# Performance work log

Hardware: AMD Instinct MI355X
Metric: run time of the kernel (lower is better)

## Reference

```python
import jax, jax.numpy as jnp
import numpy as np

N = 50000
E = 1600000
IN_DIM = 256
HID = 128
EPS = 1e-5


def _bn(x, gamma, beta):
    # BatchNorm1d forward in training mode: biased batch stats
    mean = jnp.mean(x, axis=0)
    var = jnp.mean((x - mean) ** 2, axis=0)
    return (x - mean) * jax.lax.rsqrt(var + EPS) * gamma + beta


def _sage(x, edge_index, Wl, bl, Wr):
    # PyG SAGEConv with mean aggregation:
    #   out = lin_l(mean_{j in N(i)} x_j) + lin_r(x_i)
    src, dst = edge_index[0], edge_index[1]
    agg = jax.ops.segment_sum(x[src], dst, num_segments=N)          # [N, H]
    cnt = jax.ops.segment_sum(jnp.ones((src.shape[0],), x.dtype), dst, num_segments=N)
    mean = agg / jnp.maximum(cnt, 1.0)[:, None]
    return mean @ Wl + bl + x @ Wr


def setup_inputs() -> dict:
    key = jax.random.key(0)
    ks = jax.random.split(key, 16)
    s_in = 1.0 / np.sqrt(IN_DIM)
    s_h = 1.0 / np.sqrt(HID)
    return {
        "x": jax.random.normal(ks[0], (N, IN_DIM), jnp.float32),
        "edge_index": jax.random.randint(ks[1], (2, E), 0, N, jnp.int32),
        # input_linear: Linear(IN_DIM, HID) + BN
        "W_in": jax.random.uniform(ks[2], (IN_DIM, HID), jnp.float32, -s_in, s_in),
        "b_in": jax.random.uniform(ks[3], (HID,), jnp.float32, -s_in, s_in),
        "g1": jnp.ones((HID,), jnp.float32), "be1": jnp.zeros((HID,), jnp.float32),
        # hidden_linear: Linear(HID, HID) + BN
        "W_hid": jax.random.uniform(ks[4], (HID, HID), jnp.float32, -s_h, s_h),
        "b_hid": jax.random.uniform(ks[5], (HID,), jnp.float32, -s_h, s_h),
        "g2": jnp.ones((HID,), jnp.float32), "be2": jnp.zeros((HID,), jnp.float32),
        # graph_conv1: SAGEConv(HID, HID) + BN
        "Wl1": jax.random.uniform(ks[6], (HID, HID), jnp.float32, -s_h, s_h),
        "bl1": jax.random.uniform(ks[7], (HID,), jnp.float32, -s_h, s_h),
        "Wr1": jax.random.uniform(ks[8], (HID, HID), jnp.float32, -s_h, s_h),
        "g3": jnp.ones((HID,), jnp.float32), "be3": jnp.zeros((HID,), jnp.float32),
        # graph_conv2: SAGEConv(HID, HID) + BN
        "Wl2": jax.random.uniform(ks[9], (HID, HID), jnp.float32, -s_h, s_h),
        "bl2": jax.random.uniform(ks[10], (HID,), jnp.float32, -s_h, s_h),
        "Wr2": jax.random.uniform(ks[11], (HID, HID), jnp.float32, -s_h, s_h),
        "g4": jnp.ones((HID,), jnp.float32), "be4": jnp.zeros((HID,), jnp.float32),
    }


def reference(x, edge_index, W_in, b_in, g1, be1, W_hid, b_hid, g2, be2,
              Wl1, bl1, Wr1, g3, be3, Wl2, bl2, Wr2, g4, be4):
    feat = jax.nn.relu(_bn(x @ W_in + b_in, g1, be1))
    feat = jax.nn.relu(_bn(feat @ W_hid + b_hid, g2, be2))
    out = _bn(_sage(feat, edge_index, Wl1, bl1, Wr1), g3, be3)
    out = _bn(_sage(out, edge_index, Wl2, bl2, Wr2), g4, be4)
    return (feat, out)
```

## Files before the change

kernel.cpp:

```cpp
#include <hip/hip_runtime.h>
#include <stdint.h>

#define NN 50000
#define EE 1600000
#define IN_DIMC 256
#define HIDC 128
#define EPSC 1e-5f

#define NB 196
#define GA 512
#define CHUNK 3125
#define STILE_SHIFT 13
#define NKEY 2048

typedef unsigned short ushort_t;
typedef __attribute__((ext_vector_type(8))) short short8;
typedef __attribute__((ext_vector_type(4))) float floatx4;

static __device__ inline ushort_t f2bf(float f) {
    unsigned int u = __float_as_uint(f);
    u = u + 0x7fffu + ((u >> 16) & 1u);
    return (ushort_t)(u >> 16);
}
static __device__ inline unsigned int pack2(float a, float b) {
    return (unsigned int)f2bf(a) | ((unsigned int)f2bf(b) << 16);
}
static __device__ inline float bf2f(unsigned int bits16) {
    return __uint_as_float(bits16 << 16);
}

__global__ __launch_bounds__(256) void tcvt_all_kernel(
    const float* __restrict__ W_in, const float* __restrict__ W_hid,
    const float* __restrict__ Wl1, const float* __restrict__ Wr1,
    const float* __restrict__ Wl2, const float* __restrict__ Wr2,
    ushort_t* __restrict__ Wt_in, ushort_t* __restrict__ Wt_hid,
    ushort_t* __restrict__ Wtl1, ushort_t* __restrict__ Wtr1,
    ushort_t* __restrict__ Wtl2, ushort_t* __restrict__ Wtr2)
{
    const int idx = blockIdx.x * 256 + threadIdx.x;
    if (idx < 32768) {
        const int n = idx >> 8;
        const int k = idx & 255;
        Wt_in[idx] = f2bf(W_in[(size_t)k * 128 + n]);
    } else if (idx < 32768 + 5 * 16384) {
        const int r = idx - 32768;
        const int seg = r / 16384;
        const int j = r - seg * 16384;
        const int n = j >> 7;
        const int k = j & 127;
        const float* W; ushort_t* Wt;
        switch (seg) {
            case 0: W = W_hid; Wt = Wt_hid; break;
            case 1: W = Wl1;  Wt = Wtl1;  break;
            case 2: W = Wr1;  Wt = Wtr1;  break;
            case 3: W = Wl2;  Wt = Wtl2;  break;
            default: W = Wr2; Wt = Wtr2;  break;
        }
        Wt[j] = f2bf(W[(size_t)k * 128 + n]);
    }
}

__global__ __launch_bounds__(256) void mfma_gemm_kernel(
    const void* __restrict__ A1, const ushort_t* __restrict__ Wt1, int K1, int a1type,
    const void* __restrict__ A2, const ushort_t* __restrict__ Wt2, int K2,
    const float* __restrict__ bias, float* __restrict__ C, int M,
    const float* __restrict__ preStats, const float* __restrict__ preG,
    const float* __restrict__ preBe, float* __restrict__ outStats)
{
    __shared__ ushort_t Bs[128 * 136];
    __shared__ __align__(16) float aArr[128], bArr[128];
    __shared__ float red_s[4][128], red_q[4][128];

    const int t    = threadIdx.x;
    const int lane = t & 63;
    const int wave = t >> 6;
    const int quad = lane >> 4;
    const int l15  = lane & 15;
    const int row0 = blockIdx.x * 128 + wave * 32;
    const int doAffine = (preStats != nullptr);

    if (doAffine && t < 128) {
        const float invM = 1.0f / (float)M;
        const float mean = preStats[t] * invM;
        float var = preStats[128 + t] * invM - mean * mean;
        if (var < 0.0f) var = 0.0f;
        const float s = preG[t] / sqrtf(var + EPSC);
        aArr[t] = s;
        bArr[t] = preBe[t] - mean * s;
    }
    if (doAffine) __syncthreads();

    floatx4 acc[2][8];
    #pragma unroll
    for (int i = 0; i < 2; i++)
        #pragma unroll
        for (int j = 0; j < 8; j++)
            acc[i][j] = (floatx4){0.0f, 0.0f, 0.0f, 0.0f};

    const int ksq = quad * 8;
    bool firstChunk = true;

    for (int s = 0; s < 2; s++) {
        const void*     A     = s ? A2  : A1;
        const ushort_t* Wt    = s ? Wt2 : Wt1;
        const int       K     = s ? K2  : K1;
        const int       atype = s ? 1   : a1type;
        if (A == nullptr) continue;

        for (int kc = 0; kc < K; kc += 128) {
            if (!firstChunk) __syncthreads();
            firstChunk = false;

            #pragma unroll
            for (int p = 0; p < 8; p++) {
                const int idx = p * 256 + t;
                const int n   = idx >> 4;
                const int c0  = (idx & 15) * 8;
                *(uint4*)(Bs + n * 136 + c0) =
                    *(const uint4*)(Wt + (size_t)n * K + kc + c0);
            }
            __syncthreads();

            short8 afrag[2][4];
            if (atype == 1) {
                const ushort_t* Ab = (const ushort_t*)A;
                #pragma unroll
                for (int mt = 0; mt < 2; mt++) {
                    int gr = row0 + mt * 16 + l15;
                    if (gr > M - 1) gr = M - 1;
                    const size_t base = (size_t)gr * K + kc + ksq;
                    #pragma unroll
                    for (int ks = 0; ks < 4; ks++)
                        afrag[mt][ks] = *(const short8*)(Ab + base + ks * 32);
                }
            } else {
                const float* Af = (const float*)A;
                #pragma unroll
                for (int mt = 0; mt < 2; mt++) {
                    int gr = row0 + mt * 16 + l15;
                    if (gr > M - 1) gr = M - 1;
                    const size_t base = (size_t)gr * K + kc + ksq;
                    #pragma unroll
                    for (int ks = 0; ks < 4; ks++) {
                        float4 v0 = *(const float4*)(Af + base + ks * 32);
                        float4 v1 = *(const float4*)(Af + base + ks * 32 + 4);
                        if (doAffine && s == 0) {
                            const int k0 = ks * 32 + ksq;
                            const float4 sa0 = *(const float4*)(aArr + k0);
                            const float4 sb0 = *(const float4*)(bArr + k0);
                            const float4 sa1 = *(const float4*)(aArr + k0 + 4);
                            const float4 sb1 = *(const float4*)(bArr + k0 + 4);
                            v0.x = fmaxf(sa0.x * v0.x + sb0.x, 0.0f);
                            v0.y = fmaxf(sa0.y * v0.y + sb0.y, 0.0f);
                            v0.z = fmaxf(sa0.z * v0.z + sb0.z, 0.0f);
                            v0.w = fmaxf(sa0.w * v0.w + sb0.w, 0.0f);
                            v1.x = fmaxf(sa1.x * v1.x + sb1.x, 0.0f);
                            v1.y = fmaxf(sa1.y * v1.y + sb1.y, 0.0f);
                            v1.z = fmaxf(sa1.z * v1.z + sb1.z, 0.0f);
                            v1.w = fmaxf(sa1.w * v1.w + sb1.w, 0.0f);
                        }
                        uint4 w;
                        w.x = pack2(v0.x, v0.y);
                        w.y = pack2(v0.z, v0.w);
                        w.z = pack2(v1.x, v1.y);
                        w.w = pack2(v1.z, v1.w);
                        afrag[mt][ks] = __builtin_bit_cast(short8, w);
                    }
                }
            }

            #pragma unroll
            for (int ks = 0; ks < 4; ks++) {
                const int ko = ks * 32 + ksq;
                short8 b[8];
                #pragma unroll
                for (int j = 0; j < 8; j++)
                    b[j] = *(const short8*)(Bs + (j * 16 + l15) * 136 + ko);
                #pragma unroll
                for (int mt = 0; mt < 2; mt++) {
                    #pragma unroll
                    for (int j = 0; j < 8; j++)
                        acc[mt][j] = __builtin_amdgcn_mfma_f32_16x16x32_bf16(
                            afrag[mt][ks], b[j], acc[mt][j], 0, 0, 0);
                }
            }
        }
    }

    float s_[8], q_[8];
    #pragma unroll
    for (int j = 0; j < 8; j++) { s_[j] = 0.0f; q_[j] = 0.0f; }

    #pragma unroll
    for (int j = 0; j < 8; j++) {
        const int col = j * 16 + l15;
        const float bv = bias[col];
        #pragma unroll
        for (int mt = 0; mt < 2; mt++) {
            const int rbase = row0 + mt * 16 + quad * 4;
            #pragma unroll
            for (int reg = 0; reg < 4; reg++) {
                const float val = acc[mt][j][reg] + bv;
                const int r_ = rbase + reg;
                if (r_ < M) {
                    C[(size_t)r_ * HIDC + col] = val;
                    s_[j] += val;
                    q_[j] += val * val;
                }
            }
        }
    }
    #pragma unroll
    for (int j = 0; j < 8; j++) {
        s_[j] += __shfl_xor(s_[j], 16, 64);
        s_[j] += __shfl_xor(s_[j], 32, 64);
        q_[j] += __shfl_xor(q_[j], 16, 64);
        q_[j] += __shfl_xor(q_[j], 32, 64);
    }
    if (quad == 0) {
        #pragma unroll
        for (int j = 0; j < 8; j++) {
            red_s[wave][j * 16 + l15] = s_[j];
            red_q[wave][j * 16 + l15] = q_[j];
        }
    }
    __syncthreads();
    if (t < 128) {
        const float S = red_s[0][t] + red_s[1][t] + red_s[2][t] + red_s[3][t];
        const float Q = red_q[0][t] + red_q[1][t] + red_q[2][t] + red_q[3][t];
        atomicAdd(&outStats[t], S);
        atomicAdd(&outStats[128 + t], Q);
    }
}

__global__ __launch_bounds__(256) void bn_apply_kernel(
    const float* __restrict__ src, float* __restrict__ dstF,
    ushort_t* __restrict__ dstB, const float* __restrict__ stats,
    const float* __restrict__ gamma, const float* __restrict__ beta,
    int relu, int M)
{
    __shared__ float sc[128], sh[128];
    const int t = threadIdx.x;
    if (t < 128) {
        const float invM = 1.0f / (float)M;
        const float mean = stats[t] * invM;
        float var = stats[128 + t] * invM - mean * mean;
        if (var < 0.0f) var = 0.0f;
        const float s = gamma[t] / sqrtf(var + EPSC);
        sc[t] = s;
        sh[t] = beta[t] - mean * s;
    }
    __syncthreads();

    const int total4 = M * HIDC / 4;
    for (int i = blockIdx.x * 256 + t; i < total4; i += gridDim.x * 256) {
        float4 v = ((const float4*)src)[i];
        const int c = (i * 4) & 127;
        v.x = v.x * sc[c]     + sh[c];
        v.y = v.y * sc[c + 1] + sh[c + 1];
        v.z = v.z * sc[c + 2] + sh[c + 2];
        v.w = v.w * sc[c + 3] + sh[c + 3];
        if (relu) {
            v.x = fmaxf(v.x, 0.0f); v.y = fmaxf(v.y, 0.0f);
            v.z = fmaxf(v.z, 0.0f); v.w = fmaxf(v.w, 0.0f);
        }
        if (dstF) ((float4*)dstF)[i] = v;
        if (dstB) {
            uint2 w;
            w.x = pack2(v.x, v.y);
            w.y = pack2(v.z, v.w);
            *(uint2*)(dstB + (size_t)i * 4) = w;
        }
    }
}

__global__ __launch_bounds__(256) void bucket_hist_kernel(
    const int* __restrict__ dstArr, int* __restrict__ hist2D)
{
    __shared__ int hist[NB];
    const int t = threadIdx.x;
    for (int i = t; i < NB; i += 256) hist[i] = 0;
    __syncthreads();
    const int e0 = blockIdx.x * CHUNK;
    const int e1 = e0 + CHUNK;
    for (int e = e0 + t; e < e1; e += 256)
        atomicAdd(&hist[dstArr[e] >> 8], 1);
    __syncthreads();
    for (int i = t; i < NB; i += 256)
        hist2D[(size_t)i * GA + blockIdx.x] = hist[i];
}

__global__ __launch_bounds__(256) void bucket_offsets_kernel(
    int* __restrict__ hist2D, int* __restrict__ bucketBase, int* __restrict__ rowp)
{
    __shared__ int wtot[4];
    const int t = threadIdx.x;
    int tot = 0;
    if (t < NB) {
        int4* p = (int4*)(hist2D + (size_t)t * GA);
        int s = 0;
        for (int i = 0; i < GA / 4; i++) {
            int4 h = p[i];
            int4 o;
            o.x = s; s += h.x;
            o.y = s; s += h.y;
            o.z = s; s += h.z;
            o.w = s; s += h.w;
            p[i] = o;
        }
        tot = s;
    }
    const int lane = t & 63, w = t >> 6;
    int x = tot;
    #pragma unroll
    for (int off = 1; off < 64; off <<= 1) {
        const int y = __shfl_up(x, off);
        if (lane >= off) x += y;
    }
    if (lane == 63) wtot[w] = x;
    __syncthreads();
    int woff = 0;
    #pragma unroll
    for (int j = 0; j < 4; j++) if (j < w) woff += wtot[j];
    const int excl = x + woff - tot;
    if (t < NB) bucketBase[t] = excl;
    if (t == 0) { bucketBase[NB] = EE; rowp[NN] = EE; }
}

__global__ __launch_bounds__(256) void bucket_scatter_kernel(
    const int* __restrict__ srcArr, const int* __restrict__ dstArr,
    const int* __restrict__ hist2D, const int* __restrict__ bucketBase,
    int2* __restrict__ ebuf)
{
    __shared__ int cur[NB];
    const int t = threadIdx.x;
    for (int i = t; i < NB; i += 256)
        cur[i] = bucketBase[i] + hist2D[(size_t)i * GA + blockIdx.x];
    __syncthreads();
    const int e0 = blockIdx.x * CHUNK;
    const int e1 = e0 + CHUNK;
    for (int e = e0 + t; e < e1; e += 256) {
        const int d = dstArr[e];
        const int s = srcArr[e];
        const int p = atomicAdd(&cur[d >> 8], 1);
        ebuf[p] = make_int2(s, d);
    }
}

__global__ __launch_bounds__(256) void fine_sort_kernel(
    const int2* __restrict__ ebuf, const int* __restrict__ bucketBase,
    int* __restrict__ rowp, int* __restrict__ col)
{
    __shared__ int cnt[NKEY];
    __shared__ int wtot[4];
    const int b = blockIdx.x;
    const int t = threadIdx.x;
    const int bb0 = bucketBase[b];
    const int bb1 = bucketBase[b + 1];
    #pragma unroll
    for (int i = 0; i < 8; i++) cnt[t * 8 + i] = 0;
    __syncthreads();
    for (int e = bb0 + t; e < bb1; e += 256) {
        const int2 sd = ebuf[e];
        const int key = ((sd.y & 255) << 3) | (sd.x >> STILE_SHIFT);
        atomicAdd(&cnt[key], 1);
    }
    __syncthreads();
    int loc[8];
    int tot = 0;
    #pragma unroll
    for (int i = 0; i < 8; i++) { loc[i] = tot; tot += cnt[t * 8 + i]; }
    const int lane = t & 63, w = t >> 6;
    int x = tot;
    #pragma unroll
    for (int off = 1; off < 64; off <<= 1) {
        const int y = __shfl_up(x, off);
        if (lane >= off) x += y;
    }
    if (lane == 63) wtot[w] = x;
    __syncthreads();
    int woff = 0;
    #pragma unroll
    for (int j = 0; j < 4; j++) if (j < w) woff += wtot[j];
    const int excl = x + woff - tot;
    const int node = b * 256 + t;
    if (node < NN) rowp[node] = bb0 + excl;
    __syncthreads();
    #pragma unroll
    for (int i = 0; i < 8; i++) cnt[t * 8 + i] = excl + loc[i];
    __syncthreads();
    for (int e = bb0 + t; e < bb1; e += 256) {
        const int2 sd = ebuf[e];
        const int key = ((sd.y & 255) << 3) | (sd.x >> STILE_SHIFT);
        const int p = atomicAdd(&cnt[key], 1);
        col[bb0 + p] = sd.x;
    }
}

__global__ __launch_bounds__(256) void agg_kernel(
    const ushort_t* __restrict__ F, const int* __restrict__ row_ptr,
    const int* __restrict__ col, ushort_t* __restrict__ Mout)
{
    const int lane = threadIdx.x & 63;
    const int wave = blockIdx.x * (blockDim.x >> 6) + (threadIdx.x >> 6);
    const int nwaves = gridDim.x * (blockDim.x >> 6);
    const int coff = lane * 2;

    for (int n = wave; n < NN; n += nwaves) {
        const int b = __builtin_amdgcn_readfirstlane(row_ptr[n]);
        const int e = __builtin_amdgcn_readfirstlane(row_ptr[n + 1]);
        const int deg = e - b;
        float accx = 0.0f, accy = 0.0f;
        int j = b;
        for (; j + 8 <= e; j += 8) {
            const int s0 = col[j + 0];
            const int s1 = col[j + 1];
            const int s2 = col[j + 2];
            const int s3 = col[j + 3];
            const int s4 = col[j + 4];
            const int s5 = col[j + 5];
            const int s6 = col[j + 6];
            const int s7 = col[j + 7];
            const unsigned int v0 = *(const unsigned int*)(F + (size_t)s0 * HIDC + coff);
            const unsigned int v1 = *(const unsigned int*)(F + (size_t)s1 * HIDC + coff);
            const unsigned int v2 = *(const unsigned int*)(F + (size_t)s2 * HIDC + coff);
            const unsigned int v3 = *(const unsigned int*)(F + (size_t)s3 * HIDC + coff);
            const unsigned int v4 = *(const unsigned int*)(F + (size_t)s4 * HIDC + coff);
            const unsigned int v5 = *(const unsigned int*)(F + (size_t)s5 * HIDC + coff);
            const unsigned int v6 = *(const unsigned int*)(F + (size_t)s6 * HIDC + coff);
            const unsigned int v7 = *(const unsigned int*)(F + (size_t)s7 * HIDC + coff);
            accx += bf2f(v0 & 0xffffu) + bf2f(v1 & 0xffffu) + bf2f(v2 & 0xffffu)
                  + bf2f(v3 & 0xffffu) + bf2f(v4 & 0xffffu) + bf2f(v5 & 0xffffu)
                  + bf2f(v6 & 0xffffu) + bf2f(v7 & 0xffffu);
            accy += bf2f(v0 >> 16) + bf2f(v1 >> 16) + bf2f(v2 >> 16)
                  + bf2f(v3 >> 16) + bf2f(v4 >> 16) + bf2f(v5 >> 16)
                  + bf2f(v6 >> 16) + bf2f(v7 >> 16);
        }
        for (; j < e; j++) {
            const int s = col[j];
            const unsigned int v = *(const unsigned int*)(F + (size_t)s * HIDC + coff);
            accx += bf2f(v & 0xffffu);
            accy += bf2f(v >> 16);
        }
        const float inv = 1.0f / (float)(deg > 1 ? deg : 1);
        *(unsigned int*)(Mout + (size_t)n * HIDC + coff) =
            pack2(accx * inv, accy * inv);
    }
}

extern "C" void kernel_launch(void* const* d_in, const int* in_sizes, int n_in,
                              void* d_out, int out_size, void* d_ws, size_t ws_size,
                              hipStream_t stream)
{
    const float* x     = (const float*)d_in[0];
    const int*   ei    = (const int*)  d_in[1];
    const float* W_in  = (const float*)d_in[2];
    const float* b_in  = (const float*)d_in[3];
    const float* g1    = (const float*)d_in[4];
    const float* be1   = (const float*)d_in[5];
    const float* W_hid = (const float*)d_in[6];
    const float* b_hid = (const float*)d_in[7];
    const float* g2    = (const float*)d_in[8];
    const float* be2   = (const float*)d_in[9];
    const float* Wl1   = (const float*)d_in[10];
    const float* bl1   = (const float*)d_in[11];
    const float* Wr1   = (const float*)d_in[12];
    const float* g3    = (const float*)d_in[13];
    const float* be3   = (const float*)d_in[14];
    const float* Wl2   = (const float*)d_in[15];
    const float* bl2   = (const float*)d_in[16];
    const float* Wr2   = (const float*)d_in[17];
    const float* g4    = (const float*)d_in[18];
    const float* be4   = (const float*)d_in[19];

    const int* srcArr = ei;
    const int* dstArr = ei + EE;

    char* ws = (char*)d_ws;
    float*    bufA      = (float*)ws;    ws += (size_t)NN * HIDC * sizeof(float);
    float*    bufB      = (float*)ws;    ws += (size_t)NN * HIDC * sizeof(float);
    ushort_t* featB16   = (ushort_t*)ws; ws += (size_t)NN * HIDC * sizeof(ushort_t);
    ushort_t* o3B16     = (ushort_t*)ws; ws += (size_t)NN * HIDC * sizeof(ushort_t);
    ushort_t* aggB16    = (ushort_t*)ws; ws += (size_t)NN * HIDC * sizeof(ushort_t);
    float*    stats     = (float*)ws;    ws += 4 * 256 * sizeof(float);
    int*      hist2D    = (int*)ws;      ws += (size_t)NB * GA * sizeof(int);
    int*      bucketBase= (int*)ws;      ws += (NB + 4) * sizeof(int);
    int*      rowp      = (int*)ws;      ws += (size_t)(NN + 4) * sizeof(int);
    int*      colIdx    = (int*)ws;      ws += (size_t)EE * sizeof(int);
    int2*     ebuf      = (int2*)ws;     ws += (size_t)EE * sizeof(int2);
    ushort_t* Wt_in     = (ushort_t*)ws; ws += 128 * 256 * sizeof(ushort_t);
    ushort_t* Wt_hid    = (ushort_t*)ws; ws += 128 * 128 * sizeof(ushort_t);
    ushort_t* Wtl1      = (ushort_t*)ws; ws += 128 * 128 * sizeof(ushort_t);
    ushort_t* Wtr1      = (ushort_t*)ws; ws += 128 * 128 * sizeof(ushort_t);
    ushort_t* Wtl2      = (ushort_t*)ws; ws += 128 * 128 * sizeof(ushort_t);
    ushort_t* Wtr2      = (ushort_t*)ws; ws += 128 * 128 * sizeof(ushort_t);

    float* out0 = (float*)d_out;
    float* out1 = out0 + (size_t)NN * HIDC;

    hipMemsetAsync(stats, 0, 4 * 256 * sizeof(float), stream);

    tcvt_all_kernel<<<448, 256, 0, stream>>>(W_in, W_hid, Wl1, Wr1, Wl2, Wr2,
                                             Wt_in, Wt_hid, Wtl1, Wtr1, Wtl2, Wtr2);

    bucket_hist_kernel<<<GA, 256, 0, stream>>>(dstArr, hist2D);
    bucket_offsets_kernel<<<1, 256, 0, stream>>>(hist2D, bucketBase, rowp);
    bucket_scatter_kernel<<<GA, 256, 0, stream>>>(srcArr, dstArr, hist2D,
                                                  bucketBase, ebuf);
    fine_sort_kernel<<<NB, 256, 0, stream>>>(ebuf, bucketBase, rowp, colIdx);

    const int gemmGrid = (NN + 127) / 128;

    mfma_gemm_kernel<<<gemmGrid, 256, 0, stream>>>(
        x, Wt_in, IN_DIMC, 0, nullptr, nullptr, 0,
        b_in, bufA, NN, nullptr, nullptr, nullptr, stats + 0);

    mfma_gemm_kernel<<<gemmGrid, 256, 0, stream>>>(
        bufA, Wt_hid, HIDC, 0, nullptr, nullptr, 0,
        b_hid, bufB, NN, stats + 0, g1, be1, stats + 256);

    bn_apply_kernel<<<1024, 256, 0, stream>>>(bufB, out0, featB16,
                                              stats + 256, g2, be2, 1, NN);

    agg_kernel<<<4096, 256, 0, stream>>>(featB16, rowp, colIdx, aggB16);
    mfma_gemm_kernel<<<gemmGrid, 256, 0, stream>>>(
        aggB16, Wtl1, HIDC, 1, featB16, Wtr1, HIDC,
        bl1, bufA, NN, nullptr, nullptr, nullptr, stats + 512);

    bn_apply_kernel<<<1024, 256, 0, stream>>>(bufA, nullptr, o3B16,
                                              stats + 512, g3, be3, 0, NN);

    agg_kernel<<<4096, 256, 0, stream>>>(o3B16, rowp, colIdx, aggB16);
    mfma_gemm_kernel<<<gemmGrid, 256, 0, stream>>>(
        aggB16, Wtl2, HIDC, 1, o3B16, Wtr2, HIDC,
        bl2, bufB, NN, nullptr, nullptr, nullptr, stats + 768);

    bn_apply_kernel<<<1024, 256, 0, stream>>>(bufB, out1, nullptr,
                                              stats + 768, g4, be4, 0, NN);
}
```

Baseline: 441.5 us.

## Shrink GEMM tiles, drop LDS B staging, pack edges and intermediates to 16-bit

The GEMM now processes 64 rows per block with one 16-row tile per wave. It reads weight fragments directly from global memory instead of staging them through shared memory, which removes the block barriers. The first GEMM writes a bf16 intermediate, and the second GEMM applies BN+ReLU on the bf16 input, which halves that round-trip traffic at some precision cost. Edge buffers pack src/dst into 32 bits and column indices into 16-bit shorts; this relies on N fitting in 16 bits. The aggregation kernel now launches one wave per node instead of a grid-stride loop.

```diff
diff --git a/kernel.cpp b/kernel.cpp
--- a/kernel.cpp
+++ b/kernel.cpp
@@ -60,14 +60,14 @@
     }
 }
 
-__global__ __launch_bounds__(256) void mfma_gemm_kernel(
+__global__ __launch_bounds__(256, 4) void mfma_gemm_kernel(
     const void* __restrict__ A1, const ushort_t* __restrict__ Wt1, int K1, int a1type,
     const void* __restrict__ A2, const ushort_t* __restrict__ Wt2, int K2,
-    const float* __restrict__ bias, float* __restrict__ C, int M,
+    const float* __restrict__ bias, float* __restrict__ Cf, ushort_t* __restrict__ Cb,
+    int M,
     const float* __restrict__ preStats, const float* __restrict__ preG,
     const float* __restrict__ preBe, float* __restrict__ outStats)
 {
-    __shared__ ushort_t Bs[128 * 136];
     __shared__ __align__(16) float aArr[128], bArr[128];
     __shared__ float red_s[4][128], red_q[4][128];
 
@@ -76,29 +76,30 @@
     const int wave = t >> 6;
     const int quad = lane >> 4;
     const int l15  = lane & 15;
-    const int row0 = blockIdx.x * 128 + wave * 32;
+    const int row0 = blockIdx.x * 64 + wave * 16;
     const int doAffine = (preStats != nullptr);
 
-    if (doAffine && t < 128) {
-        const float invM = 1.0f / (float)M;
-        const float mean = preStats[t] * invM;
-        float var = preStats[128 + t] * invM - mean * mean;
-        if (var < 0.0f) var = 0.0f;
-        const float s = preG[t] / sqrtf(var + EPSC);
-        aArr[t] = s;
-        bArr[t] = preBe[t] - mean * s;
-    }
-    if (doAffine) __syncthreads();
-
-    floatx4 acc[2][8];
-    #pragma unroll
-    for (int i = 0; i < 2; i++)
-        #pragma unroll
-        for (int j = 0; j < 8; j++)
-            acc[i][j] = (floatx4){0.0f, 0.0f, 0.0f, 0.0f};
+    if (doAffine) {
+        if (t < 128) {
+            const float invM = 1.0f / (float)M;
+            const float mean = preStats[t] * invM;
+            float var = preStats[128 + t] * invM - mean * mean;
+            if (var < 0.0f) var = 0.0f;
+            const float s = preG[t] / sqrtf(var + EPSC);
+            aArr[t] = s;
+            bArr[t] = preBe[t] - mean * s;
+        }
+        __syncthreads();
+    }
+
+    floatx4 acc[8];
+    #pragma unroll
+    for (int j = 0; j < 8; j++)
+        acc[j] = (floatx4){0.0f, 0.0f, 0.0f, 0.0f};
 
     const int ksq = quad * 8;
-    bool firstChunk = true;
+    int gr = row0 + l15;
+    if (gr > M - 1) gr = M - 1;
 
     for (int s = 0; s < 2; s++) {
         const void*     A     = s ? A2  : A1;
@@ -108,81 +109,74 @@
         if (A == nullptr) continue;
 
         for (int kc = 0; kc < K; kc += 128) {
-            if (!firstChunk) __syncthreads();
-            firstChunk = false;
-
-            #pragma unroll
-            for (int p = 0; p < 8; p++) {
-                const int idx = p * 256 + t;
-                const int n   = idx >> 4;
-                const int c0  = (idx & 15) * 8;
-                *(uint4*)(Bs + n * 136 + c0) =
-                    *(const uint4*)(Wt + (size_t)n * K + kc + c0);
-            }
-            __syncthreads();
-
-            short8 afrag[2][4];
+            short8 afrag[4];
             if (atype == 1) {
                 const ushort_t* Ab = (const ushort_t*)A;
+                const size_t base = (size_t)gr * K + kc + ksq;
                 #pragma unroll
-                for (int mt = 0; mt < 2; mt++) {
-                    int gr = row0 + mt * 16 + l15;
-                    if (gr > M - 1) gr = M - 1;
-                    const size_t base = (size_t)gr * K + kc + ksq;
+                for (int ks = 0; ks < 4; ks++)
+                    afrag[ks] = *(const short8*)(Ab + base + ks * 32);
+                if (doAffine && s == 0) {
                     #pragma unroll
-                    for (int ks = 0; ks < 4; ks++)
-                        afrag[mt][ks] = *(const short8*)(Ab + base + ks * 32);
+                    for (int ks = 0; ks < 4; ks++) {
+                        const int k0 = kc + ks * 32 + ksq;
+                        uint4 u = __builtin_bit_cast(uint4, afrag[ks]);
+                        uint4 w;
+                        unsigned int* up = (unsigned int*)&u;
+                        unsigned int* wp = (unsigned int*)&w;
+                        #pragma unroll
+                        for (int h = 0; h < 4; h++) {
+                            const float lo = bf2f(up[h] & 0xffffu);
+                            const float hi = bf2f(up[h] >> 16);
+                            const float flo = fmaxf(aArr[k0 + h * 2]     * lo + bArr[k0 + h * 2],     0.0f);
+                            const float fhi = fmaxf(aArr[k0 + h * 2 + 1] * hi + bArr[k0 + h * 2 + 1], 0.0f);
+                            wp[h] = pack2(flo, fhi);
+                        }
+                        afrag[ks] = __builtin_bit_cast(short8, w);
+                    }
                 }
             } else {
                 const float* Af = (const float*)A;
+                const size_t base = (size_t)gr * K + kc + ksq;
                 #pragma unroll
-                for (int mt = 0; mt < 2; mt++) {
-                    int gr = row0 + mt * 16 + l15;
-                    if (gr > M - 1) gr = M - 1;
-                    const size_t base = (size_t)gr * K + kc + ksq;
-                    #pragma unroll
-                    for (int ks = 0; ks < 4; ks++) {
-                        float4 v0 = *(const float4*)(Af + base + ks * 32);
-                        float4 v1 = *(const float4*)(Af + base + ks * 32 + 4);
-                        if (doAffine && s == 0) {
-                            const int k0 = ks * 32 + ksq;
-                            const float4 sa0 = *(const float4*)(aArr + k0);
-                            const float4 sb0 = *(const float4*)(bArr + k0);
-                            const float4 sa1 = *(const float4*)(aArr + k0 + 4);
-                            const float4 sb1 = *(const float4*)(bArr + k0 + 4);
-                            v0.x = fmaxf(sa0.x * v0.x + sb0.x, 0.0f);
-                            v0.y = fmaxf(sa0.y * v0.y + sb0.y, 0.0f);
-                            v0.z = fmaxf(sa0.z * v0.z + sb0.z, 0.0f);
-                            v0.w = fmaxf(sa0.w * v0.w + sb0.w, 0.0f);
-                            v1.x = fmaxf(sa1.x * v1.x + sb1.x, 0.0f);
-                            v1.y = fmaxf(sa1.y * v1.y + sb1.y, 0.0f);
-                            v1.z = fmaxf(sa1.z * v1.z + sb1.z, 0.0f);
-                            v1.w = fmaxf(sa1.w * v1.w + sb1.w, 0.0f);
-                        }
-                        uint4 w;
-                        w.x = pack2(v0.x, v0.y);
-                        w.y = pack2(v0.z, v0.w);
-                        w.z = pack2(v1.x, v1.y);
-                        w.w = pack2(v1.z, v1.w);
-                        afrag[mt][ks] = __builtin_bit_cast(short8, w);
+                for (int ks = 0; ks < 4; ks++) {
+                    float4 v0 = *(const float4*)(Af + base + ks * 32);
+                    float4 v1 = *(const float4*)(Af + base + ks * 32 + 4);
+                    if (doAffine && s == 0) {
+                        const int k0 = kc + ks * 32 + ksq;
+                        const float4 sa0 = *(const float4*)(aArr + k0);
+                        const float4 sb0 = *(const float4*)(bArr + k0);
+                        const float4 sa1 = *(const float4*)(aArr + k0 + 4);
+                        const float4 sb1 = *(const float4*)(bArr + k0 + 4);
+                        v0.x = fmaxf(sa0.x * v0.x + sb0.x, 0.0f);
+                        v0.y = fmaxf(sa0.y * v0.y + sb0.y, 0.0f);
+                        v0.z = fmaxf(sa0.z * v0.z + sb0.z, 0.0f);
+                        v0.w = fmaxf(sa0.w * v0.w + sb0.w, 0.0f);
+                        v1.x = fmaxf(sa1.x * v1.x + sb1.x, 0.0f);
+                        v1.y = fmaxf(sa1.y * v1.y + sb1.y, 0.0f);
+                        v1.z = fmaxf(sa1.z * v1.z + sb1.z, 0.0f);
+                        v1.w = fmaxf(sa1.w * v1.w + sb1.w, 0.0f);
                     }
+                    uint4 w;
+                    w.x = pack2(v0.x, v0.y);
+                    w.y = pack2(v0.z, v0.w);
+                    w.z = pack2(v1.x, v1.y);
+                    w.w = pack2(v1.z, v1.w);
+                    afrag[ks] = __builtin_bit_cast(short8, w);
                 }
             }
 
             #pragma unroll
             for (int ks = 0; ks < 4; ks++) {
-                const int ko = ks * 32 + ksq;
+                const int ko = kc + ks * 32 + ksq;
                 short8 b[8];
                 #pragma unroll
                 for (int j = 0; j < 8; j++)
-                    b[j] = *(const short8*)(Bs + (j * 16 + l15) * 136 + ko);
+                    b[j] = *(const short8*)(Wt + (size_t)(j * 16 + l15) * K + ko);
                 #pragma unroll
-                for (int mt = 0; mt < 2; mt++) {
-                    #pragma unroll
-                    for (int j = 0; j < 8; j++)
-                        acc[mt][j] = __builtin_amdgcn_mfma_f32_16x16x32_bf16(
-                            afrag[mt][ks], b[j], acc[mt][j], 0, 0, 0);
-                }
+                for (int j = 0; j < 8; j++)
+                    acc[j] = __builtin_amdgcn_mfma_f32_16x16x32_bf16(
+                        afrag[ks], b[j], acc[j], 0, 0, 0);
             }
         }
     }
@@ -195,18 +189,16 @@
     for (int j = 0; j < 8; j++) {
         const int col = j * 16 + l15;
         const float bv = bias[col];
+        const int rbase = row0 + quad * 4;
         #pragma unroll
-        for (int mt = 0; mt < 2; mt++) {
-            const int rbase = row0 + mt * 16 + quad * 4;
-            #pragma unroll
-            for (int reg = 0; reg < 4; reg++) {
-                const float val = acc[mt][j][reg] + bv;
-                const int r_ = rbase + reg;
-                if (r_ < M) {
-                    C[(size_t)r_ * HIDC + col] = val;
-                    s_[j] += val;
-                    q_[j] += val * val;
-                }
+        for (int reg = 0; reg < 4; reg++) {
+            const float val = acc[j][reg] + bv;
+            const int r_ = rbase + reg;
+            if (r_ < M) {
+                if (Cf) Cf[(size_t)r_ * HIDC + col] = val;
+                if (Cb) Cb[(size_t)r_ * HIDC + col] = f2bf(val);
+                s_[j] += val;
+                q_[j] += val * val;
             }
         }
     }
@@ -330,7 +322,7 @@
 __global__ __launch_bounds__(256) void bucket_scatter_kernel(
     const int* __restrict__ srcArr, const int* __restrict__ dstArr,
     const int* __restrict__ hist2D, const int* __restrict__ bucketBase,
-    int2* __restrict__ ebuf)
+    unsigned int* __restrict__ ebuf)
 {
     __shared__ int cur[NB];
     const int t = threadIdx.x;
@@ -343,13 +335,13 @@
         const int d = dstArr[e];
         const int s = srcArr[e];
         const int p = atomicAdd(&cur[d >> 8], 1);
-        ebuf[p] = make_int2(s, d);
+        ebuf[p] = ((unsigned int)s << 16) | (unsigned int)d;
     }
 }
 
 __global__ __launch_bounds__(256) void fine_sort_kernel(
-    const int2* __restrict__ ebuf, const int* __restrict__ bucketBase,
-    int* __restrict__ rowp, int* __restrict__ col)
+    const unsigned int* __restrict__ ebuf, const int* __restrict__ bucketBase,
+    int* __restrict__ rowp, ushort_t* __restrict__ col)
 {
     __shared__ int cnt[NKEY];
     __shared__ int wtot[4];
@@ -361,8 +353,8 @@
     for (int i = 0; i < 8; i++) cnt[t * 8 + i] = 0;
     __syncthreads();
     for (int e = bb0 + t; e < bb1; e += 256) {
-        const int2 sd = ebuf[e];
-        const int key = ((sd.y & 255) << 3) | (sd.x >> STILE_SHIFT);
+        const unsigned int sd = ebuf[e];
+        const int key = (int)((sd & 255u) << 3) | (int)(sd >> (16 + STILE_SHIFT));
         atomicAdd(&cnt[key], 1);
     }
     __syncthreads();
@@ -390,62 +382,47 @@
     for (int i = 0; i < 8; i++) cnt[t * 8 + i] = excl + loc[i];
     __syncthreads();
     for (int e = bb0 + t; e < bb1; e += 256) {
-        const int2 sd = ebuf[e];
-        const int key = ((sd.y & 255) << 3) | (sd.x >> STILE_SHIFT);
+        const unsigned int sd = ebuf[e];
+        const int key = (int)((sd & 255u) << 3) | (int)(sd >> (16 + STILE_SHIFT));
         const int p = atomicAdd(&cnt[key], 1);
-        col[bb0 + p] = sd.x;
+        col[bb0 + p] = (ushort_t)(sd >> 16);
     }
 }
 
 __global__ __launch_bounds__(256) void agg_kernel(
     const ushort_t* __restrict__ F, const int* __restrict__ row_ptr,
-    const int* __restrict__ col, ushort_t* __restrict__ Mout)
+    const ushort_t* __restrict__ col, ushort_t* __restrict__ Mout)
 {
     const int lane = threadIdx.x & 63;
-    const int wave = blockIdx.x * (blockDim.x >> 6) + (threadIdx.x >> 6);
-    const int nwaves = gridDim.x * (blockDim.x >> 6);
+    const int n = blockIdx.x * 4 + (threadIdx.x >> 6);
     const int coff = lane * 2;
 
-    for (int n = wave; n < NN; n += nwaves) {
-        const int b = __builtin_amdgcn_readfirstlane(row_ptr[n]);
-        const int e = __builtin_amdgcn_readfirstlane(row_ptr[n + 1]);
-        const int deg = e - b;
-        float accx = 0.0f, accy = 0.0f;
-        int j = b;
-        for (; j + 8 <= e; j += 8) {
-            const int s0 = col[j + 0];
-            const int s1 = col[j + 1];
-            const int s2 = col[j + 2];
-            const int s3 = col[j + 3];
-            const int s4 = col[j + 4];
-            const int s5 = col[j + 5];
-            const int s6 = col[j + 6];
-            const int s7 = col[j + 7];
-            const unsigned int v0 = *(const unsigned int*)(F + (size_t)s0 * HIDC + coff);
-            const unsigned int v1 = *(const unsigned int*)(F + (size_t)s1 * HIDC + coff);
-            const unsigned int v2 = *(const unsigned int*)(F + (size_t)s2 * HIDC + coff);
-            const unsigned int v3 = *(const unsigned int*)(F + (size_t)s3 * HIDC + coff);
-            const unsigned int v4 = *(const unsigned int*)(F + (size_t)s4 * HIDC + coff);
-            const unsigned int v5 = *(const unsigned int*)(F + (size_t)s5 * HIDC + coff);
-            const unsigned int v6 = *(const unsigned int*)(F + (size_t)s6 * HIDC + coff);
-            const unsigned int v7 = *(const unsigned int*)(F + (size_t)s7 * HIDC + coff);
-            accx += bf2f(v0 & 0xffffu) + bf2f(v1 & 0xffffu) + bf2f(v2 & 0xffffu)
-                  + bf2f(v3 & 0xffffu) + bf2f(v4 & 0xffffu) + bf2f(v5 & 0xffffu)
-                  + bf2f(v6 & 0xffffu) + bf2f(v7 & 0xffffu);
-            accy += bf2f(v0 >> 16) + bf2f(v1 >> 16) + bf2f(v2 >> 16)
-                  + bf2f(v3 >> 16) + bf2f(v4 >> 16) + bf2f(v5 >> 16)
-                  + bf2f(v6 >> 16) + bf2f(v7 >> 16);
-        }
-        for (; j < e; j++) {
-            const int s = col[j];
-            const unsigned int v = *(const unsigned int*)(F + (size_t)s * HIDC + coff);
-            accx += bf2f(v & 0xffffu);
-            accy += bf2f(v >> 16);
-        }
-        const float inv = 1.0f / (float)(deg > 1 ? deg : 1);
-        *(unsigned int*)(Mout + (size_t)n * HIDC + coff) =
-            pack2(accx * inv, accy * inv);
-    }
+    const int b = __builtin_amdgcn_readfirstlane(row_ptr[n]);
+    const int e = __builtin_amdgcn_readfirstlane(row_ptr[n + 1]);
+    const int deg = e - b;
+    float accx = 0.0f, accy = 0.0f;
+    int j = b;
+    for (; j + 8 <= e; j += 8) {
+        int s0[8];
+        #pragma unroll
+        for (int i = 0; i < 8; i++) s0[i] = col[j + i];
+        unsigned int v0[8];
+        #pragma unroll
+        for (int i = 0; i < 8; i++)
+            v0[i] = *(const unsigned int*)(F + (size_t)s0[i] * HIDC + coff);
+        #pragma unroll
+        for (int i = 0; i < 8; i++) {
+            accx += bf2f(v0[i] & 0xffffu);
+            accy += bf2f(v0[i] >> 16);
+        }
+    }
+    for (; j < e; j++) {
+        const unsigned int v = *(const unsigned int*)(F + (size_t)col[j] * HIDC + coff);
+        accx += bf2f(v & 0xffffu);
+        accy += bf2f(v >> 16);
+    }
+    const float inv = 1.0f / (float)(deg > 1 ? deg : 1);
+    *(unsigned int*)(Mout + (size_t)n * HIDC + coff) = pack2(accx * inv, accy * inv);
 }
 
 extern "C" void kernel_launch(void* const* d_in, const int* in_sizes, int n_in,
@@ -479,6 +456,7 @@
     char* ws = (char*)d_ws;
     float*    bufA      = (float*)ws;    ws += (size_t)NN * HIDC * sizeof(float);
     float*    bufB      = (float*)ws;    ws += (size_t)NN * HIDC * sizeof(float);
+    ushort_t* bufA16    = (ushort_t*)ws; ws += (size_t)NN * HIDC * sizeof(ushort_t);
     ushort_t* featB16   = (ushort_t*)ws; ws += (size_t)NN * HIDC * sizeof(ushort_t);
     ushort_t* o3B16     = (ushort_t*)ws; ws += (size_t)NN * HIDC * sizeof(ushort_t);
     ushort_t* aggB16    = (ushort_t*)ws; ws += (size_t)NN * HIDC * sizeof(ushort_t);
@@ -486,8 +464,8 @@
     int*      hist2D    = (int*)ws;      ws += (size_t)NB * GA * sizeof(int);
     int*      bucketBase= (int*)ws;      ws += (NB + 4) * sizeof(int);
     int*      rowp      = (int*)ws;      ws += (size_t)(NN + 4) * sizeof(int);
-    int*      colIdx    = (int*)ws;      ws += (size_t)EE * sizeof(int);
-    int2*     ebuf      = (int2*)ws;     ws += (size_t)EE * sizeof(int2);
+    ushort_t* colIdx    = (ushort_t*)ws; ws += (size_t)EE * sizeof(ushort_t) + 64;
+    unsigned int* ebuf  = (unsigned int*)ws; ws += (size_t)EE * sizeof(unsigned int);
     ushort_t* Wt_in     = (ushort_t*)ws; ws += 128 * 256 * sizeof(ushort_t);
     ushort_t* Wt_hid    = (ushort_t*)ws; ws += 128 * 128 * sizeof(ushort_t);
     ushort_t* Wtl1      = (ushort_t*)ws; ws += 128 * 128 * sizeof(ushort_t);
@@ -509,31 +487,31 @@
                                                   bucketBase, ebuf);
     fine_sort_kernel<<<NB, 256, 0, stream>>>(ebuf, bucketBase, rowp, colIdx);
 
-    const int gemmGrid = (NN + 127) / 128;
+    const int gemmGrid = (NN + 63) / 64;
 
     mfma_gemm_kernel<<<gemmGrid, 256, 0, stream>>>(
         x, Wt_in, IN_DIMC, 0, nullptr, nullptr, 0,
-        b_in, bufA, NN, nullptr, nullptr, nullptr, stats + 0);
+        b_in, nullptr, bufA16, NN, nullptr, nullptr, nullptr, stats + 0);
 
     mfma_gemm_kernel<<<gemmGrid, 256, 0, stream>>>(
-        bufA, Wt_hid, HIDC, 0, nullptr, nullptr, 0,
-        b_hid, bufB, NN, stats + 0, g1, be1, stats + 256);
+        bufA16, Wt_hid, HIDC, 1, nullptr, nullptr, 0,
+        b_hid, bufB, nullptr, NN, stats + 0, g1, be1, stats + 256);
 
     bn_apply_kernel<<<1024, 256, 0, stream>>>(bufB, out0, featB16,
                                               stats + 256, g2, be2, 1, NN);
 
-    agg_kernel<<<4096, 256, 0, stream>>>(featB16, rowp, colIdx, aggB16);
+    agg_kernel<<<12500, 256, 0, stream>>>(featB16, rowp, colIdx, aggB16);
     mfma_gemm_kernel<<<gemmGrid, 256, 0, stream>>>(
         aggB16, Wtl1, HIDC, 1, featB16, Wtr1, HIDC,
-        bl1, bufA, NN, nullptr, nullptr, nullptr, stats + 512);
+        bl1, bufA, nullptr, NN, nullptr, nullptr, nullptr, stats + 512);
 
     bn_apply_kernel<<<1024, 256, 0, stream>>>(bufA, nullptr, o3B16,
                                               stats + 512, g3, be3, 0, NN);
 
-    agg_kernel<<<4096, 256, 0, stream>>>(o3B16, rowp, colIdx, aggB16);
+    agg_kernel<<<12500, 256, 0, stream>>>(o3B16, rowp, colIdx, aggB16);
     mfma_gemm_kernel<<<gemmGrid, 256, 0, stream>>>(
         aggB16, Wtl2, HIDC, 1, o3B16, Wtr2, HIDC,
-        bl2, bufB, NN, nullptr, nullptr, nullptr, stats + 768);
+        bl2, bufB, nullptr, NN, nullptr, nullptr, nullptr, stats + 768);
 
     bn_apply_kernel<<<1024, 256, 0, stream>>>(bufB, out1, nullptr,
                                               stats + 768, g4, be4, 0, NN);
```

Measured after the change: 541.8 us. 22.7% more time.
